# Performance work log

Measured on AMD Instinct MI355X. Metric: run time of the kernel, lower is better.

## Reference

```python
import jax, jax.numpy as jnp
import numpy as np

B, L, DM, E, N, R, S = 2, 1024, 512, 1024, 16, 32, 64
BN_SCALE = float(1.0 / np.sqrt(1.0 + 1e-5))  # eval-mode BatchNorm1d with default running stats


def _ssm(x, Wx, bx, Wdt, bdt, A_log, D):
    # x: [B,L,E] -> Mamba selective scan output [B,L,E]
    dbc = x @ Wx.T + bx                                   # [B,L,R+2N]
    delta = jax.nn.softplus(dbc[..., :R] @ Wdt.T + bdt)   # [B,L,E]
    Bm = dbc[..., R:R + N]                                # [B,L,N]
    Cm = dbc[..., R + N:]                                 # [B,L,N]
    A = -jnp.exp(A_log)                                   # [E,N]
    dA = jnp.exp(delta[..., None] * A)                    # [B,L,E,N]
    dBx = delta[..., None] * Bm[:, :, None, :] * x[..., None]

    def comb(c1, c2):
        a1, b1 = c1
        a2, b2 = c2
        return a1 * a2, b1 * a2 + b2

    _, h = jax.lax.associative_scan(comb, (dA, dBx), axis=1)  # [B,L,E,N]
    return jnp.einsum('blen,bln->ble', h, Cm) + D * x


def _gmask_idx(length, batch):
    ref = (length + 1) // 2
    idx = jnp.arange(length, dtype=jnp.float32)
    sigma = jnp.abs(idx - ref).mean()
    w = jnp.exp(-0.5 * (idx - ref) ** 2 / sigma ** 2)
    w = w / w.sum()
    return jnp.broadcast_to(w, (batch, length))


def _gmask_vec(seq):
    length = seq.shape[1]
    ref = seq[:, (length + 1) // 2, :]
    d = jnp.linalg.norm(seq - ref[:, None, :], axis=2)    # [B,L]
    sigma = d.mean(axis=1, keepdims=True)
    w = jnp.exp(-0.5 * (d / sigma) ** 2)
    return w / w.sum(axis=1, keepdims=True)


def _spatial_attn(x, w, b):
    # x: [B,L,C]; SpatialAttention: returns weighted map in [B,C,L] layout
    xt = jnp.swapaxes(x, 1, 2)                            # [B,C,L]
    fmap = (w[0] * xt.max(axis=1) + w[1] * xt.mean(axis=1) + b) * BN_SCALE
    wmap = jax.nn.sigmoid(jax.nn.relu(fmap))[:, None, :]  # [B,1,L]
    return xt * wmap                                      # [B,C,L]


def _forward(x, W_in_x, b_in_x, W_in_z, b_in_z, convf_w, convf_b, convb_w, convb_b,
             Wx_f, bx_f, Wdt_f, bdt_f, A_log_f, D_f,
             Wx_b, bx_b, Wdt_b, bdt_b, A_log_b, D_b,
             W_cat, b_cat, sa_w, sa_b, wA_f, wV_f,
             W_proj, b_proj, W_Bi, b_Bi, tf_w, tf_b, W_out, b_out):
    b_, l_, _ = x.shape
    xi = x @ W_in_x.T + b_in_x                            # [B,L,E]
    z = x @ W_in_z.T + b_in_z                             # [B,L,E]
    # depthwise conv1d with kernel_size=1 == per-channel affine
    x_f = jax.nn.silu(xi * convf_w + convf_b)
    x_b = jax.nn.silu(jnp.flip(xi, axis=1) * convb_w + convb_b)
    y_f = jnp.tanh(_ssm(x_f, Wx_f, bx_f, Wdt_f, bdt_f, A_log_f, D_f))
    y_b = jnp.tanh(_ssm(x_b, Wx_b, bx_b, Wdt_b, bdt_b, A_log_b, D_b))
    gi = _gmask_idx(l_, b_)
    mf = jax.nn.softmax(gi * _gmask_vec(y_f), axis=1)
    mb = jax.nn.softmax(gi * _gmask_vec(y_b), axis=1)
    y_cat = jnp.concatenate([y_f * mf[..., None],
                             y_b * jnp.flip(mb[..., None], axis=1)], axis=-1)
    y = y_cat @ W_cat.T + b_cat                           # [B,L,E]
    m = jax.nn.softmax(gi * _gmask_vec(y_cat), axis=1)
    y = y * m[..., None]
    yw = _spatial_attn(y, sa_w, sa_b)                     # [B,E,L]
    y = jnp.swapaxes(yw, 1, 2)                            # [B,L,E]
    # STL tokenizer (forward direction weights)
    Aw = jax.nn.softmax(jnp.swapaxes(y @ wA_f.T, 1, 2), axis=-1)  # [B,S,L]
    u = Aw @ (y @ wV_f)                                   # [B,S,E]
    # z branch: adaptive average pool L -> S (L % S == 0), then SiLU
    zp = jax.nn.silu(jnp.swapaxes(z, 1, 2).reshape(b_, E, S, l_ // S).mean(-1))
    zt = jnp.swapaxes(zp, 1, 2)                           # [B,S,E]
    # TokenFuser -- faithful to original's .view-based memory reinterpretation
    Y = (u.reshape(b_, E, S) @ W_proj.T + b_proj).reshape(b_, S, E)
    Bw = jax.nn.sigmoid(zt @ W_Bi.T + b_Bi)               # [B,S,S]
    BwY = Bw @ Y                                          # [B,S,E]
    xj = _spatial_attn(zt, tf_w, tf_b).reshape(b_, S, E)  # view (reshape), not transpose
    out = BwY + xj
    return jnp.tanh(out @ W_out.T + b_out)                # [B,S,DM]


def setup_inputs():
    ks = jax.random.split(jax.random.key(0), 24)
    g = lambda i, shape, s=0.02: jax.random.normal(ks[i], shape, dtype=jnp.float32) * s
    A_log = jnp.log(jnp.tile(jnp.arange(1, N + 1, dtype=jnp.float32), (E, 1)))
    return dict(
        x=jax.random.normal(ks[0], (B, L, DM), dtype=jnp.float32),
        W_in_x=g(1, (E, DM)), b_in_x=jnp.zeros((E,), jnp.float32),
        W_in_z=g(2, (E, DM)), b_in_z=jnp.zeros((E,), jnp.float32),
        convf_w=1.0 + g(3, (E,)), convf_b=jnp.zeros((E,), jnp.float32),
        convb_w=1.0 + g(4, (E,)), convb_b=jnp.zeros((E,), jnp.float32),
        Wx_f=g(5, (R + 2 * N, E)), bx_f=jnp.zeros((R + 2 * N,), jnp.float32),
        Wdt_f=g(6, (E, R)), bdt_f=jnp.full((E,), -4.0, jnp.float32),
        A_log_f=A_log, D_f=jnp.ones((E,), jnp.float32),
        Wx_b=g(7, (R + 2 * N, E)), bx_b=jnp.zeros((R + 2 * N,), jnp.float32),
        Wdt_b=g(8, (E, R)), bdt_b=jnp.full((E,), -4.0, jnp.float32),
        A_log_b=A_log, D_b=jnp.ones((E,), jnp.float32),
        W_cat=g(9, (E, 2 * E)), b_cat=jnp.zeros((E,), jnp.float32),
        sa_w=g(10, (2,), 0.5), sa_b=jnp.zeros((), jnp.float32),
        wA_f=g(11, (S, E), 0.05), wV_f=g(12, (E, E), 0.02),
        W_proj=g(13, (S, S), 0.1), b_proj=jnp.zeros((S,), jnp.float32),
        W_Bi=g(14, (S, E)), b_Bi=jnp.zeros((S,), jnp.float32),
        tf_w=g(15, (2,), 0.5), tf_b=jnp.zeros((), jnp.float32),
        W_out=g(16, (DM, E)), b_out=jnp.zeros((DM,), jnp.float32),
    )


def reference(x, W_in_x, b_in_x, W_in_z, b_in_z, convf_w, convf_b, convb_w, convb_b,
              Wx_f, bx_f, Wdt_f, bdt_f, A_log_f, D_f,
              Wx_b, bx_b, Wdt_b, bdt_b, A_log_b, D_b,
              W_cat, b_cat, sa_w, sa_b, wA_f, wV_f,
              W_proj, b_proj, W_Bi, b_Bi, tf_w, tf_b, W_out, b_out):
    return _forward(x, W_in_x, b_in_x, W_in_z, b_in_z, convf_w, convf_b, convb_w, convb_b,
                    Wx_f, bx_f, Wdt_f, bdt_f, A_log_f, D_f,
                    Wx_b, bx_b, Wdt_b, bdt_b, A_log_b, D_b,
                    W_cat, b_cat, sa_w, sa_b, wA_f, wV_f,
                    W_proj, b_proj, W_Bi, b_Bi, tf_w, tf_b, W_out, b_out)
```

## Files before the change

### kernel.cpp

```cpp
#include <hip/hip_runtime.h>
#include <math.h>

#define DEVI static __device__ __forceinline__

namespace {

constexpr float BN_SCALE_C = 0.9999950000374997f;

typedef __bf16 bf8v __attribute__((ext_vector_type(8)));
typedef float f4v __attribute__((ext_vector_type(4)));

DEVI float sigmoidf_(float x){ return 1.0f/(1.0f+expf(-x)); }
DEVI float siluf_(float x){ return x/(1.0f+expf(-x)); }
DEVI float softplusf_(float x){ return fmaxf(x,0.0f) + log1pf(__expf(-fabsf(x))); }

DEVI unsigned short f2bf(float f){
  union{float f; unsigned int u;} v; v.f=f;
  unsigned int r = v.u + 0x7fffu + ((v.u>>16)&1u);
  return (unsigned short)(r>>16);
}

DEVI float bredw_sum(float v, float* sh){
  #pragma unroll
  for (int o=32;o;o>>=1) v += __shfl_xor(v, o);
  __syncthreads();
  if ((threadIdx.x&63)==0) sh[threadIdx.x>>6] = v;
  __syncthreads();
  return sh[0]+sh[1]+sh[2]+sh[3];
}
DEVI float bredw_max(float v, float* sh){
  #pragma unroll
  for (int o=32;o;o>>=1) v = fmaxf(v, __shfl_xor(v, o));
  __syncthreads();
  if ((threadIdx.x&63)==0) sh[threadIdx.x>>6] = v;
  __syncthreads();
  return fmaxf(fmaxf(sh[0],sh[1]), fmaxf(sh[2],sh[3]));
}

DEVI void gld_lds16(const unsigned short* g, unsigned short* l){
  __builtin_amdgcn_global_load_lds(
      (const __attribute__((address_space(1))) unsigned int*)(g),
      (__attribute__((address_space(3))) unsigned int*)(l), 16, 0, 0);
}

DEVI void stage_tile64(const unsigned short* __restrict__ Ak,
                       const unsigned short* __restrict__ Bk,
                       size_t lda, size_t ldb,
                       unsigned short* As, unsigned short* Bs,
                       int w, int lane)
{
  #pragma unroll
  for (int i=0;i<2;++i){
    int seg = (w<<1) + i;
    int row = (seg<<3) + (lane>>3);
    int c   = (lane & 7) ^ (row & 7);
    gld_lds16(Ak + (size_t)row*lda + (c<<3), As + (seg<<9));
    gld_lds16(Bk + (size_t)row*ldb + (c<<3), Bs + (seg<<9));
  }
}

DEVI void gemm_core(const unsigned short* __restrict__ Ag,
                    const unsigned short* __restrict__ Bg,
                    size_t lda, size_t ldb, int ksteps,
                    unsigned short* As, unsigned short* Bs, f4v (&acc)[2][2])
{
  const int tid = threadIdx.x;
  const int lane = tid & 63, w = tid >> 6;
  const int wr = w >> 1, wc = w & 1;
  const int l15 = lane & 15, l4 = lane >> 4;

  int cur = 0;
  stage_tile64(Ag, Bg, lda, ldb, As, Bs, w, lane);
  asm volatile("s_waitcnt vmcnt(0)" ::: "memory");
  __syncthreads();
  for (int ks = 0; ks < ksteps; ++ks){
    unsigned short* Asc = As + (cur<<12);
    unsigned short* Bsc = Bs + (cur<<12);
    if (ks+1 < ksteps)
      stage_tile64(Ag + (size_t)(ks+1)*64, Bg + (size_t)(ks+1)*64, lda, ldb,
                   As + ((cur^1)<<12), Bs + ((cur^1)<<12), w, lane);
    #pragma unroll
    for (int kk=0;kk<2;++kk){
      int cb = (kk<<2) + l4;
      bf8v af[2], bfv[2];
      #pragma unroll
      for (int mi=0;mi<2;++mi){
        int row = (wr<<5)+(mi<<4)+l15;
        af[mi] = *(const bf8v*)(Asc + (row<<6) + ((cb^(row&7))<<3));
      }
      #pragma unroll
      for (int ni=0;ni<2;++ni){
        int row = (wc<<5)+(ni<<4)+l15;
        bfv[ni] = *(const bf8v*)(Bsc + (row<<6) + ((cb^(row&7))<<3));
      }
      #pragma unroll
      for (int mi=0;mi<2;++mi)
        #pragma unroll
        for (int ni=0;ni<2;++ni)
          acc[mi][ni] = __builtin_amdgcn_mfma_f32_16x16x32_bf16(af[mi], bfv[ni], acc[mi][ni], 0,0,0);
    }
    asm volatile("s_waitcnt vmcnt(0)" ::: "memory");
    __syncthreads();
    cur ^= 1;
  }
}

template<int EPI>
__global__ __launch_bounds__(256) void gemm_bf16_k(
    const unsigned short* __restrict__ A, const unsigned short* __restrict__ Bt,
    const float* __restrict__ bias, void* __restrict__ Cout,
    int N, int K,
    const unsigned short* __restrict__ Bt2, const float* __restrict__ bias2, long sC)
{
  __shared__ unsigned short As[8192], Bs[8192];
  float* Cf = (float*)Cout;
  if (Bt2 && blockIdx.z){ Bt = Bt2; bias = bias2; Cf += sC; }
  const int m0 = blockIdx.y<<6, n0 = blockIdx.x<<6;
  f4v acc[2][2] = {};
  gemm_core(A + (size_t)m0*K, Bt + (size_t)n0*K, K, K, K>>6, As, Bs, acc);
  const int lane = threadIdx.x & 63, w = threadIdx.x >> 6;
  const int wr = w>>1, wc = w&1, l15 = lane&15, l4 = lane>>4;
  #pragma unroll
  for (int mi=0;mi<2;++mi)
    #pragma unroll
    for (int ni=0;ni<2;++ni){
      int col = n0 + (wc<<5) + (ni<<4) + l15;
      float bv = bias ? bias[col] : 0.f;
      #pragma unroll
      for (int r=0;r<4;++r){
        int rowg = m0 + (wr<<5) + (mi<<4) + (l4<<2) + r;
        Cf[(size_t)rowg*N + col] = acc[mi][ni][r] + bv;
      }
    }
}

template<int EPI>
__global__ __launch_bounds__(256) void gemm_small_k(
    const unsigned short* __restrict__ A, const unsigned short* __restrict__ Bt,
    const float* __restrict__ b0, const float* __restrict__ b1,
    void* __restrict__ Cout, int N, int K, int mshift, long sB)
{
  __shared__ unsigned char smem[65536];
  unsigned short* AsAll = (unsigned short*)smem;
  unsigned short* BsAll = (unsigned short*)(smem + 32768);
  float* Lc = (float*)smem;

  const int tid = threadIdx.x;
  const int lane = tid & 63, w = tid >> 6;
  const int m0 = blockIdx.y<<6, n0 = blockIdx.x<<6;
  const unsigned short* Ab = A + (size_t)m0*K;
  const unsigned short* Bb = Bt + (size_t)(m0>>mshift)*sB + (size_t)n0*K;
  unsigned short* Asw = AsAll + (w<<12);
  unsigned short* Bsw = BsAll + (w<<12);
  const int kpw = K >> 2;
  const int nst = kpw >> 6;
  const int l15 = lane & 15, l4 = lane >> 4;
  const int srow8 = lane >> 3, sc = lane & 7;

  f4v acc[4][4] = {};
  for (int ks = 0; ks < nst; ++ks){
    const int kbase = w*kpw + (ks<<6);
    #pragma unroll
    for (int seg=0; seg<8; ++seg){
      int row = (seg<<3) + srow8;
      int c = sc ^ (row & 7);
      gld_lds16(Ab + (size_t)row*K + kbase + (c<<3), Asw + (seg<<9));
      gld_lds16(Bb + (size_t)row*K + kbase + (c<<3), Bsw + (seg<<9));
    }
    asm volatile("s_waitcnt vmcnt(0)" ::: "memory");
    #pragma unroll
    for (int kk=0; kk<2; ++kk){
      int cb = (kk<<2) + l4;
      bf8v af[4], bfv[4];
      #pragma unroll
      for (int mi=0;mi<4;++mi){
        int row = (mi<<4) + l15;
        af[mi] = *(const bf8v*)(Asw + (row<<6) + ((cb^(row&7))<<3));
      }
      #pragma unroll
      for (int ni=0;ni<4;++ni){
        int row = (ni<<4) + l15;
        bfv[ni] = *(const bf8v*)(Bsw + (row<<6) + ((cb^(row&7))<<3));
      }
      #pragma unroll
      for (int mi=0;mi<4;++mi)
        #pragma unroll
        for (int ni=0;ni<4;++ni)
          acc[mi][ni] = __builtin_amdgcn_mfma_f32_16x16x32_bf16(af[mi], bfv[ni], acc[mi][ni], 0,0,0);
    }
    __builtin_amdgcn_sched_barrier(0);
  }
  __syncthreads();
  #pragma unroll
  for (int mi=0;mi<4;++mi)
    #pragma unroll
    for (int ni=0;ni<4;++ni){
      int col = (ni<<4) + l15;
      #pragma unroll
      for (int r=0;r<4;++r){
// ... 62 lines not shown
    int tx = threadIdx.x & 31, ty = threadIdx.x >> 5;
    if (tb < 1024){
      int by = tb >> 5, bx = tb & 31;
      #pragma unroll
      for (int r=0;r<4;++r){
        int row = by*32 + ty + r*8;
        tsh[ty + r*8][tx] = wV[(long)row*1024 + bx*32 + tx];
      }
      __syncthreads();
      #pragma unroll
      for (int r=0;r<4;++r){
        int row = bx*32 + ty + r*8;
        wVT[(long)row*1024 + by*32 + tx] = f2bf(tsh[tx][ty + r*8]);
      }
    } else {
      int q = tb - 1024;
      int dir = q >> 5, bi = q & 31;
      const float* src = dir ? Wdt_b : Wdt_f;
      float* dst = WdtT + (dir<<15);
      #pragma unroll
      for (int r=0;r<4;++r){
        int row = bi*32 + ty + r*8;
        tsh[ty + r*8][tx] = src[(long)row*32 + tx];
      }
      __syncthreads();
      #pragma unroll
      for (int r=0;r<4;++r){
        int c = ty + r*8;
        dst[(long)c*1024 + bi*32 + tx] = tsh[tx][c];
      }
    }
    return;
  }
  int i = (blockIdx.x*256 + threadIdx.x)*4;
  const float* s; unsigned short* d;
  if (i < n0){ s = s0; d = d0; }
  else if ((i -= n0) < n1){ s = s1; d = d1; }
  else if ((i -= n1) < n2){ s = s2; d = d2; }
  else if ((i -= n2) < n3){ s = s3; d = d3; }
  else if ((i -= n3) < n4){ s = s4; d = d4; }
  else if ((i -= n4) < n5){ s = s5; d = d5; }
  else if ((i -= n5) < n6){ s = s6; d = d6; }
  else if ((i -= n6) < n7){ s = s7; d = d7; }
  else return;
  float4 v = *(const float4*)(s + i);
  union{ unsigned short u[4]; uint2 p; } o;
  o.u[0]=f2bf(v.x); o.u[1]=f2bf(v.y); o.u[2]=f2bf(v.z); o.u[3]=f2bf(v.w);
  *(uint2*)(d + i) = o.p;
}

__global__ __launch_bounds__(256) void convzt_k(const float* __restrict__ xi, const float* __restrict__ z,
    const float* __restrict__ cfw, const float* __restrict__ cfb,
    const float* __restrict__ cbw, const float* __restrict__ cbb,
    float* __restrict__ xf, float* __restrict__ xb, unsigned short* __restrict__ xfb_bf,
    float* __restrict__ ztb)
{
  int bx = blockIdx.x, t = threadIdx.x;
  if (bx < 2048){
    int base = (bx*256 + t) << 2;
    int e = base & 1023;
    int bl = base >> 10; int l = bl & 1023, b = bl >> 10;
    float4 cw = *(const float4*)(cfw + e);
    float4 cb = *(const float4*)(cfb + e);
    float4 xv = *(const float4*)(xi + base);
    float4 vf;
    vf.x = siluf_(fmaf(xv.x, cw.x, cb.x));
    vf.y = siluf_(fmaf(xv.y, cw.y, cb.y));
    vf.z = siluf_(fmaf(xv.z, cw.z, cb.z));
    vf.w = siluf_(fmaf(xv.w, cw.w, cb.w));
    *(float4*)(xf + base) = vf;
    union{unsigned short u[4]; uint2 p;} o;
    o.u[0]=f2bf(vf.x); o.u[1]=f2bf(vf.y); o.u[2]=f2bf(vf.z); o.u[3]=f2bf(vf.w);
    *(uint2*)(xfb_bf + base) = o.p;
    int jb = (((b<<10) + (1023-l))<<10) + e;
    float4 cw2 = *(const float4*)(cbw + e);
    float4 cb2 = *(const float4*)(cbb + e);
    float4 xw = *(const float4*)(xi + jb);
    float4 vb;
    vb.x = siluf_(fmaf(xw.x, cw2.x, cb2.x));
    vb.y = siluf_(fmaf(xw.y, cw2.y, cb2.y));
    vb.z = siluf_(fmaf(xw.z, cw2.z, cb2.z));
    vb.w = siluf_(fmaf(xw.w, cw2.w, cb2.w));
    *(float4*)(xb + base) = vb;
    union{unsigned short u[4]; uint2 p;} o2;
    o2.u[0]=f2bf(vb.x); o2.u[1]=f2bf(vb.y); o2.u[2]=f2bf(vb.z); o2.u[3]=f2bf(vb.w);
    *(uint2*)(xfb_bf + 2097152 + base) = o2.p;
  } else {
    int base = ((bx-2048)*256 + t) << 2;
    int e = base & 1023; int bs = base >> 10; int s = bs & 63; int b = bs >> 6;
    const float* zp = z + (((long)((b<<10)+(s<<4)))<<10) + e;
    float4 sm = {0.f,0.f,0.f,0.f};
    #pragma unroll
    for (int j=0;j<16;++j){
      float4 v = *(const float4*)(zp + ((long)j<<10));
      sm.x += v.x; sm.y += v.y; sm.z += v.z; sm.w += v.w;
    }
    float4 o;
    o.x = siluf_(sm.x*(1.f/16.f)); o.y = siluf_(sm.y*(1.f/16.f));
    o.z = siluf_(sm.z*(1.f/16.f)); o.w = siluf_(sm.w*(1.f/16.f));
    *(float4*)(ztb + base) = o;
  }
}

__global__ __launch_bounds__(256) void dbcdelta_k(
    const float* __restrict__ dbcF, const float* __restrict__ WdtT,
    const float* __restrict__ bdt_f, const float* __restrict__ bdt_b,
    float* __restrict__ delta)
{
  __shared__ float sdbc[8][64];
  const int t = threadIdx.x;
  const int r0 = blockIdx.x * 8;
  const int dir = r0 >> 11;
  const float* bdt = dir ? bdt_b : bdt_f;
  const float* WT  = WdtT + (dir<<15);
  for (int idx=t; idx<512; idx+=256){
    int r = idx>>6, c = idx&63;
    sdbc[r][c] = dbcF[(long)(r0+r)*64 + c];
  }
  __syncthreads();
  const int c0 = t << 2;
  float4 bv = *(const float4*)(bdt + c0);
  float4 acc[8];
  #pragma unroll
  for (int r=0;r<8;++r) acc[r] = bv;
  #pragma unroll
  for (int k=0;k<32;++k){
    float4 w = *(const float4*)(WT + (k<<10) + c0);
    #pragma unroll
    for (int r=0;r<8;++r){
      float a = sdbc[r][k];
      acc[r].x = fmaf(a, w.x, acc[r].x);
      acc[r].y = fmaf(a, w.y, acc[r].y);
      acc[r].z = fmaf(a, w.z, acc[r].z);
      acc[r].w = fmaf(a, w.w, acc[r].w);
    }
  }
  #pragma unroll
  for (int r=0;r<8;++r){
    float4 o;
    o.x = softplusf_(acc[r].x); o.y = softplusf_(acc[r].y);
    o.z = softplusf_(acc[r].z); o.w = softplusf_(acc[r].w);
    *(float4*)(delta + (long)(r0+r)*1024 + c0) = o;
  }
}

__global__ __launch_bounds__(256) void ssm_chunk_k(
    const float* __restrict__ xs0, const float* __restrict__ dl0,
    const float* __restrict__ dbc0, const float* __restrict__ A_log_f,
    const float* __restrict__ A_log_b,
    float* __restrict__ pA0, float* __restrict__ hend0)
{
  const int dir = blockIdx.y;
  const float* xs   = xs0  + (size_t)dir*2097152;
  const float* delta= dl0  + (size_t)dir*2097152;
  const float* dbc  = dbc0 + (size_t)dir*131072;
  const float* A_log= dir ? A_log_b : A_log_f;
  float* pA   = pA0   + (size_t)dir*1048576;
  float* hend = hend0 + (size_t)dir*1048576;

  __shared__ float sB[32][16];
  const int tid = threadIdx.x;
  const int lane = tid & 63, w = tid >> 6;
  const int le = lane & 31, half = lane >> 5;
  const int bc = blockIdx.x >> 3;
  const int b = bc >> 5, c = bc & 31;
  const int e = ((blockIdx.x & 7) << 7) + (w << 5) + le;
  for (int i=tid; i<512; i+=256){
    int l=i>>4, n=i&15;
    sB[l][n] = dbc[(((b<<10) + (c<<5) + l)<<6) + 32 + n];
  }
  __syncthreads();
  const int n0 = half << 3;
  float An[8];
  #pragma unroll
  for (int j=0;j<8;++j) An[j] = -__expf(A_log[(e<<4)+n0+j]);
  float h[8];
  #pragma unroll
  for (int j=0;j<8;++j) h[j]=0.0f;
  float ds = 0.f;
  long base = ((long)((b<<10) + (c<<5)))*1024 + e;
  for (int l=0;l<32;++l){
    float dl = delta[base + ((long)l<<10)];
    float xv = xs[base + ((long)l<<10)];
    float dx = dl*xv;
    ds += dl;
    #pragma unroll
    for (int j=0;j<8;++j){
      float a = __expf(dl*An[j]);
      h[j] = fmaf(a, h[j], dx*sB[l][n0+j]);
    }
  }
  long ob = ((long)((b<<5)+c)<<4)*1024 + e;
  #pragma unroll
  for (int j=0;j<8;++j){
    pA[ob + ((long)(n0+j)<<10)] = __expf(ds*An[j]);
    hend[ob + ((long)(n0+j)<<10)] = h[j];
  }
}

__global__ __launch_bounds__(256) void ssm_carry_k(
    const float* __restrict__ pA, const float* __restrict__ hend, float* __restrict__ Hc)
{
  int i = blockIdx.x*256 + threadIdx.x;
  int e = i & 1023, n = (i>>10)&15, b = (i>>14)&1, dir = (i>>15)&1;
  const float* pAd = pA   + (size_t)dir*1048576;
  const float* hd  = hend + (size_t)dir*1048576;
  float* Hd        = Hc   + (size_t)dir*1048576;
  float H = 0.f;
  long base = ((long)(b*512 + n))*1024 + e;
  for (int c=0;c<32;++c){
    long a = base + (long)c*16384;
    Hd[a] = H;
    H = fmaf(pAd[a], H, hd[a]);
  }
}

__global__ __launch_bounds__(256) void ssm_out_k(
    const float* __restrict__ xs0, const float* __restrict__ dl0,
    const float* __restrict__ dbc0, const float* __restrict__ A_log_f,
    const float* __restrict__ A_log_b, const float* __restrict__ Hc0,
    const float* __restrict__ D_f, const float* __restrict__ D_b,
    float* __restrict__ y0)
{
  const int dir = blockIdx.y;
  const float* xs   = xs0  + (size_t)dir*2097152;
  const float* delta= dl0  + (size_t)dir*2097152;
  const float* dbc  = dbc0 + (size_t)dir*131072;
  const float* A_log= dir ? A_log_b : A_log_f;
  const float* Hc   = Hc0 + (size_t)dir*1048576;
  const float* D    = dir ? D_b : D_f;
  float* y          = y0 + (size_t)dir*2097152;

  __shared__ float sB[32][16], sC[32][16];
  const int tid = threadIdx.x;
  const int lane = tid & 63, w = tid >> 6;
  const int le = lane & 31, half = lane >> 5;
  const int bc = blockIdx.x >> 3;
  const int b = bc >> 5, c = bc & 31;
  const int e = ((blockIdx.x & 7) << 7) + (w << 5) + le;
  for (int i=tid;i<512;i+=256){
    int l=i>>4, n=i&15;
    int bbase = ((b<<10)+(c<<5)+l)<<6;
    sB[l][n] = dbc[bbase+32+n];
    sC[l][n] = dbc[bbase+48+n];
  }
  __syncthreads();
  const int n0 = half << 3;
  float An[8], h[8];
  long ib = ((long)((b<<5)+c)<<4)*1024 + e;
  #pragma unroll
  for(int j=0;j<8;++j){
    An[j] = -__expf(A_log[(e<<4)+n0+j]);
    h[j] = Hc[ib+((long)(n0+j)<<10)];
  }
  const float Dv = D[e];
  long base = ((long)((b<<10)+(c<<5)))*1024 + e;
  for (int l=0;l<32;++l){
    float dl = delta[base+((long)l<<10)];
    float xv = xs[base+((long)l<<10)];
    float dx = dl*xv;
    float acc = half ? 0.f : Dv*xv;
    #pragma unroll
    for(int j=0;j<8;++j){
      float a = __expf(dl*An[j]);
      h[j] = fmaf(a,h[j],dx*sB[l][n0+j]);
      acc = fmaf(h[j], sC[l][n0+j], acc);
    }
    acc += __shfl_xor(acc, 32);
    if (!half) y[base+((long)l<<10)] = tanhf(acc);
  }
}

__global__ __launch_bounds__(256) void stats_k(const float* __restrict__ y,
    float* __restrict__ nrm, float* __restrict__ dotv)
{
  __shared__ float sh[4];
  int row = blockIdx.x;
  int rowref = (row & ~1023) + 512;
  const float4* rp  = (const float4*)(y + (long)row*1024);
  const float4* rf  = (const float4*)(y + (long)rowref*1024);
  float4 a = rp[threadIdx.x], r = rf[threadIdx.x];
  float sn = a.x*a.x + a.y*a.y + a.z*a.z + a.w*a.w;
  float sd = a.x*r.x + a.y*r.y + a.z*r.z + a.w*r.w;
  sn = bredw_sum(sn, sh);
  sd = bredw_sum(sd, sh);
  if (threadIdx.x==0){ nrm[row] = sn; dotv[row] = sd; }
}

DEVI void softmask(const float (&d)[4], const float (&gi)[4], float gsum,
                   float* sh, float (&m)[4])
{
  float s = d[0]+d[1]+d[2]+d[3];
  float sig = bredw_sum(s, sh) * (1.0f/1024.0f);
  float inv = 1.0f/sig;
  float w[4]; s = 0.f;
  #pragma unroll
  for (int i=0;i<4;++i){ float r = d[i]*inv; w[i] = __expf(-0.5f*r*r); s += w[i]; }
  float wsm = bredw_sum(s, sh);
  float sc = 1.0f/(wsm*gsum);
  float tv[4]; float mx = -1e30f;
  #pragma unroll
  for (int i=0;i<4;++i){ tv[i] = gi[i]*w[i]*sc; mx = fmaxf(mx, tv[i]); }
  mx = bredw_max(mx, sh);
  s = 0.f;
  #pragma unroll
  for (int i=0;i<4;++i){ tv[i] = __expf(tv[i]-mx); s += tv[i]; }
  float es = bredw_sum(s, sh);
  float ie = 1.0f/es;
  #pragma unroll
  for (int i=0;i<4;++i) m[i] = tv[i]*ie;
}

__global__ __launch_bounds__(256) void mask2_k(
    const float* __restrict__ nrm, const float* __restrict__ dotv,
    float* __restrict__ mfG, float* __restrict__ mbG, float* __restrict__ mvG)
{
  __shared__ float mfs[1024], mbs[1024], sh[4];
  const int b = blockIdx.x, t = threadIdx.x;
  const float nf512 = nrm[(b<<10)+512];
  const float nb512 = nrm[2048+(b<<10)+512];
  float gi[4], nf[4], pf[4], nb[4], pb[4];
  float gs = 0.f;
  #pragma unroll
  for (int i=0;i<4;++i){
    int l = t + (i<<8);
    float q = (float)(l-512) * (1.0f/256.0f);
    gi[i] = __expf(-0.5f*q*q); gs += gi[i];
    nf[i] = nrm[(b<<10)+l];      pf[i] = dotv[(b<<10)+l];
    nb[i] = nrm[2048+(b<<10)+l]; pb[i] = dotv[2048+(b<<10)+l];
  }
  float gsum = bredw_sum(gs, sh);
  float mf[4], mb[4], d[4];
  #pragma unroll
  for (int i=0;i<4;++i) d[i] = sqrtf(fmaxf(nf[i] - 2.f*pf[i] + nf512, 0.f));
  softmask(d, gi, gsum, sh, mf);
  #pragma unroll
  for (int i=0;i<4;++i) d[i] = sqrtf(fmaxf(nb[i] - 2.f*pb[i] + nb512, 0.f));
  softmask(d, gi, gsum, sh, mb);
  #pragma unroll
  for (int i=0;i<4;++i){
    int l = t + (i<<8);
    mfs[l] = mf[i]; mbs[l] = mb[i];
    mfG[(b<<10)+l] = mf[i]; mbG[(b<<10)+l] = mb[i];
  }
  __syncthreads();
  const float mf512 = mfs[512], mb511 = mbs[511];
  #pragma unroll
  for (int i=0;i<4;++i){
    int l = t + (i<<8);
    float mbf = mbs[1023-l];
    float dc2 = mf[i]*mf[i]*nf[i] - 2.f*mf[i]*mf512*pf[i] + mf512*mf512*nf512
              + mbf*mbf*nb[i]     - 2.f*mbf*mb511*pb[i]   + mb511*mb511*nb512;
    d[i] = sqrtf(fmaxf(dc2, 0.f));
  }
  float mv[4];
  softmask(d, gi, gsum, sh, mv);
  #pragma unroll
  for (int i=0;i<4;++i) mvG[(b<<10)+t+(i<<8)] = mv[i];
}

__global__ __launch_bounds__(256) void ycat_k(const float* __restrict__ yf, const float* __restrict__ yb,
    const float* __restrict__ mf, const float* __restrict__ mb, unsigned short* __restrict__ yc)
{
  int base = (blockIdx.x*256 + threadIdx.x) << 2;
  int e = base & 1023; int bl = base >> 10; int l = bl & 1023, b = bl >> 10;
  float mfv = mf[bl];
  float mbv = mb[(b<<10) + (1023-l)];
  float4 vf = *(const float4*)(yf + base);
  float4 vb = *(const float4*)(yb + base);
  long r = (long)bl*2048;
  union{unsigned short u[4]; uint2 p;} o;
  o.u[0]=f2bf(vf.x*mfv); o.u[1]=f2bf(vf.y*mfv); o.u[2]=f2bf(vf.z*mfv); o.u[3]=f2bf(vf.w*mfv);
  *(uint2*)(yc + r + e) = o.p;
  union{unsigned short u[4]; uint2 p;} o2;
  o2.u[0]=f2bf(vb.x*mbv); o2.u[1]=f2bf(vb.y*mbv); o2.u[2]=f2bf(vb.z*mbv); o2.u[3]=f2bf(vb.w*mbv);
  *(uint2*)(yc + r + 1024 + e) = o2.p;
}

__global__ __launch_bounds__(256) void rowscale_k(const float* __restrict__ y, const float* __restrict__ m,
    const float* __restrict__ sw, const float* __restrict__ sb, unsigned short* __restrict__ yo)
{
  __shared__ float sh[4];
  int row = blockIdx.x;
  float mv = m[row];
  float4 v = ((const float4*)(y + (long)row*1024))[threadIdx.x];
  v.x *= mv; v.y *= mv; v.z *= mv; v.w *= mv;
  float mx = fmaxf(fmaxf(v.x,v.y), fmaxf(v.z,v.w));
  float sm = v.x+v.y+v.z+v.w;
  float rmax = bredw_max(mx, sh);
  float rsum = bredw_sum(sm, sh);
  float fmap = (sw[0]*rmax + sw[1]*(rsum*(1.0f/1024.0f)) + sb[0])*BN_SCALE_C;
  float sc = sigmoidf_(fmaxf(fmap, 0.0f));
  union{unsigned short u[4]; uint2 p;} o;
  o.u[0]=f2bf(v.x*sc); o.u[1]=f2bf(v.y*sc); o.u[2]=f2bf(v.z*sc); o.u[3]=f2bf(v.w*sc);
  *(uint2*)(yo + (long)row*1024 + (threadIdx.x<<2)) = o.p;
}

__global__ __launch_bounds__(256) void awsmT_k(const float* __restrict__ yA,
    unsigned short* __restrict__ Aw,
    const unsigned short* __restrict__ src, unsigned short* __restrict__ dst)
{
  __shared__ float sh[4];
  __shared__ unsigned short tsh[32][33];
  if (blockIdx.x < 128){
    int bs = blockIdx.x; int b = bs >> 6, s = bs & 63;
    float v[4]; float mx=-1e30f;
    #pragma unroll
    for(int i=0;i<4;++i){
      int l = threadIdx.x+(i<<8);
      v[i] = yA[(long)((b<<10)+l)*64 + s];
      mx = fmaxf(mx, v[i]);
    }
    mx = bredw_max(mx, sh);
    float sm=0.0f;
    #pragma unroll
    for(int i=0;i<4;++i){ v[i]=__expf(v[i]-mx); sm+=v[i]; }
    sm = bredw_sum(sm, sh);
    float inv = 1.0f/sm;
    #pragma unroll
    for(int i=0;i<4;++i){ int l=threadIdx.x+(i<<8); Aw[(((b<<6)+s)<<10)+l] = f2bf(v[i]*inv); }
  } else {
    int tb = blockIdx.x - 128;
    size_t bo = (size_t)(tb>>10) << 20;
    int rem = tb & 1023;
    int by = rem >> 5, bx = rem & 31;
    int tx = threadIdx.x & 31, ty = threadIdx.x >> 5;
    #pragma unroll
    for (int r=0;r<4;++r){
// ... 96 lines not shown

}

extern "C" void kernel_launch(void* const* d_in, const int* in_sizes, int n_in,
                              void* d_out, int out_size, void* d_ws, size_t ws_size,
                              hipStream_t stream)
{
  (void)in_sizes; (void)n_in; (void)out_size; (void)ws_size;
  const float* x      = (const float*)d_in[0];
  const float* W_in_x = (const float*)d_in[1];
  const float* b_in_x = (const float*)d_in[2];
  const float* W_in_z = (const float*)d_in[3];
  const float* b_in_z = (const float*)d_in[4];
  const float* cfw    = (const float*)d_in[5];
  const float* cfb    = (const float*)d_in[6];
  const float* cbw    = (const float*)d_in[7];
  const float* cbb    = (const float*)d_in[8];
  const float* Wx_f   = (const float*)d_in[9];
  const float* bx_f   = (const float*)d_in[10];
  const float* Wdt_f  = (const float*)d_in[11];
  const float* bdt_f  = (const float*)d_in[12];
  const float* A_log_f= (const float*)d_in[13];
  const float* D_f    = (const float*)d_in[14];
  const float* Wx_b   = (const float*)d_in[15];
  const float* bx_b   = (const float*)d_in[16];
  const float* Wdt_b  = (const float*)d_in[17];
  const float* bdt_b  = (const float*)d_in[18];
  const float* A_log_b= (const float*)d_in[19];
  const float* D_b    = (const float*)d_in[20];
  const float* W_cat  = (const float*)d_in[21];
  const float* b_cat  = (const float*)d_in[22];
  const float* sa_w   = (const float*)d_in[23];
  const float* sa_b   = (const float*)d_in[24];
  const float* wA_f   = (const float*)d_in[25];
  const float* wV_f   = (const float*)d_in[26];
  const float* W_proj = (const float*)d_in[27];
  const float* b_proj = (const float*)d_in[28];
  const float* W_Bi   = (const float*)d_in[29];
  const float* b_Bi   = (const float*)d_in[30];
  const float* tf_w   = (const float*)d_in[31];
  const float* tf_b   = (const float*)d_in[32];
  const float* W_out  = (const float*)d_in[33];
  const float* b_out  = (const float*)d_in[34];
  float* out = (float*)d_out;
  float* ws  = (float*)d_ws;

  const size_t M1 = 1u<<20;
  float* xi = ws;
  float* pA = ws;
  unsigned short* ycat_bf = (unsigned short*)ws;
  float* z = ws + 2*M1;
  float* hend = ws + 2*M1;
  float* ybufF = ws + 2*M1;
  float* xf = ws + 4*M1;
  unsigned short* ybuf_bf = (unsigned short*)(ws + 4*M1);
  float* xb = ws + 6*M1;
  unsigned short* ybufT_bf = (unsigned short*)(ws + 6*M1);
  float* yf = ws + 8*M1;
  float* yb = ws + 10*M1;
  float* u2f = ws + 10*M1;
  unsigned short* xfxb_bf = (unsigned short*)(ws + 12*M1);
  float* deltaF = ws + 12*M1;
  unsigned short* x_bf = (unsigned short*)(ws + 17*M1);
  float* Hc = ws + 16*M1;
  float* dbcF = ws + 18*M1;
  size_t woff = 18*M1 + 262144;
  unsigned short* Winx_bf = (unsigned short*)(ws + woff); woff += 262144;
  unsigned short* Winz_bf = (unsigned short*)(ws + woff); woff += 262144;
  unsigned short* Wcat_bf = (unsigned short*)(ws + woff); woff += M1;
  unsigned short* wVT_bf  = (unsigned short*)(ws + woff); woff += 524288;
  unsigned short* wA_bf   = (unsigned short*)(ws + woff); woff += 32768;
  unsigned short* Wx_bf   = (unsigned short*)(ws + woff); woff += 65536;
  unsigned short* Wout_bf = (unsigned short*)(ws + woff); woff += 262144;
  float* WdtT = ws + woff; woff += 65536;
  float* ztb  = ws + woff; woff += 131072;
  float* nrm  = ws + woff; woff += 4096;
  float* dotv = ws + woff; woff += 4096;
  float* mfG  = ws + woff; woff += 2048;
  float* mbG  = ws + woff; woff += 2048;
  float* mvG  = ws + woff; woff += 2048;
  float* gz   = ws + woff; woff += 256;
  float* yA   = ws + woff; woff += 131072;
  unsigned short* Aw_bf = (unsigned short*)(ws + woff); woff += 65536;
  unsigned short* uR_bf = (unsigned short*)(ws + woff); woff += 65536;
  float* Yp   = ws + woff; woff += 131072;
  float* Bw   = ws + woff; woff += 8192;
  unsigned short* O_bf = (unsigned short*)(ws + woff); woff += 65536;

  dim3 blk(256);

  castall_k<<<5888,blk,0,stream>>>(x, x_bf, 1048576,
                                   W_in_x, Winx_bf, 524288,
                                   W_in_z, Winz_bf, 524288,
                                   W_cat, Wcat_bf, 2097152,
                                   wA_f, wA_bf, 65536,
                                   Wx_f, Wx_bf, 65536,
                                   Wx_b, Wx_bf + 65536, 65536,
                                   W_out, Wout_bf, 524288,
                                   wV_f, wVT_bf, Wdt_f, Wdt_b, WdtT);

  gemm_bf16_k<0><<<dim3(16,32,2),blk,0,stream>>>(x_bf, Winx_bf, b_in_x, xi, 1024, 512,
                                                 Winz_bf, b_in_z, (long)(2*M1));
  convzt_k<<<2176,blk,0,stream>>>(xi, z, cfw,cfb,cbw,cbb, xf, xb, xfxb_bf, ztb);

  gemm_small_k<0><<<dim3(1,64),blk,0,stream>>>(xfxb_bf, Wx_bf, bx_f, bx_b, dbcF,
                                               64, 1024, 11, 65536);
  dbcdelta_k<<<512,blk,0,stream>>>(dbcF, WdtT, bdt_f, bdt_b, deltaF);

  ssm_chunk_k<<<dim3(512,2),blk,0,stream>>>(xf, deltaF, dbcF, A_log_f, A_log_b, pA, hend);
  ssm_carry_k<<<256,blk,0,stream>>>(pA, hend, Hc);
  ssm_out_k<<<dim3(512,2),blk,0,stream>>>(xf, deltaF, dbcF, A_log_f, A_log_b, Hc, D_f, D_b, yf);

  stats_k<<<4096,blk,0,stream>>>(yf, nrm, dotv);
  mask2_k<<<2,blk,0,stream>>>(nrm, dotv, mfG, mbG, mvG);
  ycat_k<<<2048,blk,0,stream>>>(yf, yb, mfG, mbG, ycat_bf);

  gemm_bf16_k<0><<<dim3(16,32,1),blk,0,stream>>>(ycat_bf, Wcat_bf, b_cat, ybufF, 1024, 2048,
                                                 nullptr, nullptr, 0);
  rowscale_k<<<2048,blk,0,stream>>>(ybufF, mvG, sa_w, sa_b, ybuf_bf);

  gemm_small_k<0><<<dim3(1,32),blk,0,stream>>>(ybuf_bf, wA_bf, nullptr, nullptr, yA,
                                               64, 1024, 31, 0);
  awsmT_k<<<2176,blk,0,stream>>>(yA, Aw_bf, ybuf_bf, ybufT_bf);
  gemm_small_k<1><<<dim3(16,2),blk,0,stream>>>(Aw_bf, ybufT_bf, nullptr, nullptr, uR_bf,
                                               1024, 1024, 6, (long)M1);
  gemm_small_k<0><<<dim3(16,2),blk,0,stream>>>(uR_bf, wVT_bf, nullptr, nullptr, u2f,
                                               1024, 1024, 31, 0);

  upbw_k<<<384,blk,0,stream>>>(u2f, W_proj, b_proj, ztb, W_Bi, b_Bi, tf_w, tf_b, Yp, Bw, gz);
  o_k<<<128,blk,0,stream>>>(Bw, Yp, ztb, gz, O_bf);

  gemm_small_k<2><<<dim3(8,2),blk,0,stream>>>(O_bf, Wout_bf, b_out, nullptr, out,
                                              512, 1024, 31, 0);
}
```

Measured before the change: 209.8 us.

## Store SSM intermediates in bf16 and route big GEMMs through split-K kernel

Drops the fp32 copies of the conv outputs and reuses the bf16 xf/xb buffer in the scan kernels. Delta and the scan output y are now written in bf16, and the stats and concat kernels read bf16. This roughly halves the memory traffic of those bandwidth-bound kernels, at the cost of extra rounding error in delta and y. It also removes the double-buffered 64x64 GEMM and runs the input projections and W_cat GEMM on gemm_small_k with a z-dim weight switch, which changes the tiling and split-K behaviour for these large GEMMs.

```diff
diff --git a/kernel.cpp b/kernel.cpp
--- a/kernel.cpp
+++ b/kernel.cpp
@@ -19,6 +19,10 @@
   unsigned int r = v.u + 0x7fffu + ((v.u>>16)&1u);
   return (unsigned short)(r>>16);
 }
+DEVI float bf2f(unsigned short u){
+  union{unsigned int u; float f;} v; v.u = ((unsigned int)u)<<16;
+  return v.f;
+}
 
 DEVI float bredw_sum(float v, float* sh){
   #pragma unroll
@@ -43,108 +47,19 @@
       (__attribute__((address_space(3))) unsigned int*)(l), 16, 0, 0);
 }
 
-DEVI void stage_tile64(const unsigned short* __restrict__ Ak,
-                       const unsigned short* __restrict__ Bk,
-                       size_t lda, size_t ldb,
-                       unsigned short* As, unsigned short* Bs,
-                       int w, int lane)
-{
-  #pragma unroll
-  for (int i=0;i<2;++i){
-    int seg = (w<<1) + i;
-    int row = (seg<<3) + (lane>>3);
-    int c   = (lane & 7) ^ (row & 7);
-    gld_lds16(Ak + (size_t)row*lda + (c<<3), As + (seg<<9));
-    gld_lds16(Bk + (size_t)row*ldb + (c<<3), Bs + (seg<<9));
-  }
-}
-
-DEVI void gemm_core(const unsigned short* __restrict__ Ag,
-                    const unsigned short* __restrict__ Bg,
-                    size_t lda, size_t ldb, int ksteps,
-                    unsigned short* As, unsigned short* Bs, f4v (&acc)[2][2])
-{
-  const int tid = threadIdx.x;
-  const int lane = tid & 63, w = tid >> 6;
-  const int wr = w >> 1, wc = w & 1;
-  const int l15 = lane & 15, l4 = lane >> 4;
-
-  int cur = 0;
-  stage_tile64(Ag, Bg, lda, ldb, As, Bs, w, lane);
-  asm volatile("s_waitcnt vmcnt(0)" ::: "memory");
-  __syncthreads();
-  for (int ks = 0; ks < ksteps; ++ks){
-    unsigned short* Asc = As + (cur<<12);
-    unsigned short* Bsc = Bs + (cur<<12);
-    if (ks+1 < ksteps)
-      stage_tile64(Ag + (size_t)(ks+1)*64, Bg + (size_t)(ks+1)*64, lda, ldb,
-                   As + ((cur^1)<<12), Bs + ((cur^1)<<12), w, lane);
-    #pragma unroll
-    for (int kk=0;kk<2;++kk){
-      int cb = (kk<<2) + l4;
-      bf8v af[2], bfv[2];
-      #pragma unroll
-      for (int mi=0;mi<2;++mi){
-        int row = (wr<<5)+(mi<<4)+l15;
-        af[mi] = *(const bf8v*)(Asc + (row<<6) + ((cb^(row&7))<<3));
-      }
-      #pragma unroll
-      for (int ni=0;ni<2;++ni){
-        int row = (wc<<5)+(ni<<4)+l15;
-        bfv[ni] = *(const bf8v*)(Bsc + (row<<6) + ((cb^(row&7))<<3));
-      }
-      #pragma unroll
-      for (int mi=0;mi<2;++mi)
-        #pragma unroll
-        for (int ni=0;ni<2;++ni)
-          acc[mi][ni] = __builtin_amdgcn_mfma_f32_16x16x32_bf16(af[mi], bfv[ni], acc[mi][ni], 0,0,0);
-    }
-    asm volatile("s_waitcnt vmcnt(0)" ::: "memory");
-    __syncthreads();
-    cur ^= 1;
-  }
-}
-
-template<int EPI>
-__global__ __launch_bounds__(256) void gemm_bf16_k(
-    const unsigned short* __restrict__ A, const unsigned short* __restrict__ Bt,
-    const float* __restrict__ bias, void* __restrict__ Cout,
-    int N, int K,
-    const unsigned short* __restrict__ Bt2, const float* __restrict__ bias2, long sC)
-{
-  __shared__ unsigned short As[8192], Bs[8192];
-  float* Cf = (float*)Cout;
-  if (Bt2 && blockIdx.z){ Bt = Bt2; bias = bias2; Cf += sC; }
-  const int m0 = blockIdx.y<<6, n0 = blockIdx.x<<6;
-  f4v acc[2][2] = {};
-  gemm_core(A + (size_t)m0*K, Bt + (size_t)n0*K, K, K, K>>6, As, Bs, acc);
-  const int lane = threadIdx.x & 63, w = threadIdx.x >> 6;
-  const int wr = w>>1, wc = w&1, l15 = lane&15, l4 = lane>>4;
-  #pragma unroll
-  for (int mi=0;mi<2;++mi)
-    #pragma unroll
-    for (int ni=0;ni<2;++ni){
-      int col = n0 + (wc<<5) + (ni<<4) + l15;
-      float bv = bias ? bias[col] : 0.f;
-      #pragma unroll
-      for (int r=0;r<4;++r){
-        int rowg = m0 + (wr<<5) + (mi<<4) + (l4<<2) + r;
-        Cf[(size_t)rowg*N + col] = acc[mi][ni][r] + bv;
-      }
-    }
-}
-
 template<int EPI>
 __global__ __launch_bounds__(256) void gemm_small_k(
     const unsigned short* __restrict__ A, const unsigned short* __restrict__ Bt,
     const float* __restrict__ b0, const float* __restrict__ b1,
-    void* __restrict__ Cout, int N, int K, int mshift, long sB)
+    void* __restrict__ Cout, int N, int K, int mshift, long sB,
+    const unsigned short* __restrict__ Bt2, const float* __restrict__ bias2, long sC)
 {
   __shared__ unsigned char smem[65536];
   unsigned short* AsAll = (unsigned short*)smem;
   unsigned short* BsAll = (unsigned short*)(smem + 32768);
   float* Lc = (float*)smem;
 
+  if (Bt2 && blockIdx.z){ Bt = Bt2; b0 = bias2; Cout = (void*)((float*)Cout + sC); }
   const int tid = threadIdx.x;
   const int lane = tid & 63, w = tid >> 6;
   const int m0 = blockIdx.y<<6, n0 = blockIdx.x<<6;
@@ -313,8 +228,7 @@
 __global__ __launch_bounds__(256) void convzt_k(const float* __restrict__ xi, const float* __restrict__ z,
     const float* __restrict__ cfw, const float* __restrict__ cfb,
     const float* __restrict__ cbw, const float* __restrict__ cbb,
-    float* __restrict__ xf, float* __restrict__ xb, unsigned short* __restrict__ xfb_bf,
-    float* __restrict__ ztb)
+    unsigned short* __restrict__ xfb_bf, float* __restrict__ ztb)
 {
   int bx = blockIdx.x, t = threadIdx.x;
   if (bx < 2048){
@@ -324,27 +238,21 @@
     float4 cw = *(const float4*)(cfw + e);
     float4 cb = *(const float4*)(cfb + e);
     float4 xv = *(const float4*)(xi + base);
-    float4 vf;
-    vf.x = siluf_(fmaf(xv.x, cw.x, cb.x));
-    vf.y = siluf_(fmaf(xv.y, cw.y, cb.y));
-    vf.z = siluf_(fmaf(xv.z, cw.z, cb.z));
-    vf.w = siluf_(fmaf(xv.w, cw.w, cb.w));
-    *(float4*)(xf + base) = vf;
     union{unsigned short u[4]; uint2 p;} o;
-    o.u[0]=f2bf(vf.x); o.u[1]=f2bf(vf.y); o.u[2]=f2bf(vf.z); o.u[3]=f2bf(vf.w);
+    o.u[0]=f2bf(siluf_(fmaf(xv.x, cw.x, cb.x)));
+    o.u[1]=f2bf(siluf_(fmaf(xv.y, cw.y, cb.y)));
+    o.u[2]=f2bf(siluf_(fmaf(xv.z, cw.z, cb.z)));
+    o.u[3]=f2bf(siluf_(fmaf(xv.w, cw.w, cb.w)));
     *(uint2*)(xfb_bf + base) = o.p;
     int jb = (((b<<10) + (1023-l))<<10) + e;
     float4 cw2 = *(const float4*)(cbw + e);
     float4 cb2 = *(const float4*)(cbb + e);
     float4 xw = *(const float4*)(xi + jb);
-    float4 vb;
-    vb.x = siluf_(fmaf(xw.x, cw2.x, cb2.x));
-    vb.y = siluf_(fmaf(xw.y, cw2.y, cb2.y));
-    vb.z = siluf_(fmaf(xw.z, cw2.z, cb2.z));
-    vb.w = siluf_(fmaf(xw.w, cw2.w, cb2.w));
-    *(float4*)(xb + base) = vb;
     union{unsigned short u[4]; uint2 p;} o2;
-    o2.u[0]=f2bf(vb.x); o2.u[1]=f2bf(vb.y); o2.u[2]=f2bf(vb.z); o2.u[3]=f2bf(vb.w);
+    o2.u[0]=f2bf(siluf_(fmaf(xw.x, cw2.x, cb2.x)));
+    o2.u[1]=f2bf(siluf_(fmaf(xw.y, cw2.y, cb2.y)));
+    o2.u[2]=f2bf(siluf_(fmaf(xw.z, cw2.z, cb2.z)));
+    o2.u[3]=f2bf(siluf_(fmaf(xw.w, cw2.w, cb2.w)));
     *(uint2*)(xfb_bf + 2097152 + base) = o2.p;
   } else {
     int base = ((bx-2048)*256 + t) << 2;
@@ -366,7 +274,7 @@
 __global__ __launch_bounds__(256) void dbcdelta_k(
     const float* __restrict__ dbcF, const float* __restrict__ WdtT,
     const float* __restrict__ bdt_f, const float* __restrict__ bdt_b,
-    float* __restrict__ delta)
+    unsigned short* __restrict__ delta)
 {
   __shared__ float sdbc[8][64];
   const int t = threadIdx.x;
@@ -398,22 +306,24 @@
   }
   #pragma unroll
   for (int r=0;r<8;++r){
-    float4 o;
-    o.x = softplusf_(acc[r].x); o.y = softplusf_(acc[r].y);
-    o.z = softplusf_(acc[r].z); o.w = softplusf_(acc[r].w);
-    *(float4*)(delta + (long)(r0+r)*1024 + c0) = o;
+    union{unsigned short u[4]; uint2 p;} o;
+    o.u[0] = f2bf(softplusf_(acc[r].x));
+    o.u[1] = f2bf(softplusf_(acc[r].y));
+    o.u[2] = f2bf(softplusf_(acc[r].z));
+    o.u[3] = f2bf(softplusf_(acc[r].w));
+    *(uint2*)(delta + (long)(r0+r)*1024 + c0) = o.p;
   }
 }
 
 __global__ __launch_bounds__(256) void ssm_chunk_k(
-    const float* __restrict__ xs0, const float* __restrict__ dl0,
+    const unsigned short* __restrict__ xs0, const unsigned short* __restrict__ dl0,
     const float* __restrict__ dbc0, const float* __restrict__ A_log_f,
     const float* __restrict__ A_log_b,
     float* __restrict__ pA0, float* __restrict__ hend0)
 {
   const int dir = blockIdx.y;
-  const float* xs   = xs0  + (size_t)dir*2097152;
-  const float* delta= dl0  + (size_t)dir*2097152;
+  const unsigned short* xs   = xs0 + (size_t)dir*2097152;
+  const unsigned short* delta= dl0 + (size_t)dir*2097152;
   const float* dbc  = dbc0 + (size_t)dir*131072;
   const float* A_log= dir ? A_log_b : A_log_f;
   float* pA   = pA0   + (size_t)dir*1048576;
@@ -441,8 +351,8 @@
   float ds = 0.f;
   long base = ((long)((b<<10) + (c<<5)))*1024 + e;
   for (int l=0;l<32;++l){
-    float dl = delta[base + ((long)l<<10)];
-    float xv = xs[base + ((long)l<<10)];
+    float dl = bf2f(delta[base + ((long)l<<10)]);
+    float xv = bf2f(xs[base + ((long)l<<10)]);
     float dx = dl*xv;
     ds += dl;
     #pragma unroll
@@ -477,20 +387,20 @@
 }
 
 __global__ __launch_bounds__(256) void ssm_out_k(
-    const float* __restrict__ xs0, const float* __restrict__ dl0,
+    const unsigned short* __restrict__ xs0, const unsigned short* __restrict__ dl0,
     const float* __restrict__ dbc0, const float* __restrict__ A_log_f,
     const float* __restrict__ A_log_b, const float* __restrict__ Hc0,
     const float* __restrict__ D_f, const float* __restrict__ D_b,
-    float* __restrict__ y0)
+    unsigned short* __restrict__ y0)
 {
   const int dir = blockIdx.y;
-  const float* xs   = xs0  + (size_t)dir*2097152;
-  const float* delta= dl0  + (size_t)dir*2097152;
+  const unsigned short* xs   = xs0 + (size_t)dir*2097152;
+  const unsigned short* delta= dl0 + (size_t)dir*2097152;
   const float* dbc  = dbc0 + (size_t)dir*131072;
   const float* A_log= dir ? A_log_b : A_log_f;
   const float* Hc   = Hc0 + (size_t)dir*1048576;
   const float* D    = dir ? D_b : D_f;
-  float* y          = y0 + (size_t)dir*2097152;
+  unsigned short* y = y0 + (size_t)dir*2097152;
 
   __shared__ float sB[32][16], sC[32][16];
   const int tid = threadIdx.x;
@@ -517,8 +427,8 @@
   const float Dv = D[e];
   long base = ((long)((b<<10)+(c<<5)))*1024 + e;
   for (int l=0;l<32;++l){
-    float dl = delta[base+((long)l<<10)];
-    float xv = xs[base+((long)l<<10)];
+    float dl = bf2f(delta[base+((long)l<<10)]);
+    float xv = bf2f(xs[base+((long)l<<10)]);
     float dx = dl*xv;
     float acc = half ? 0.f : Dv*xv;
     #pragma unroll
@@ -528,21 +438,25 @@
       acc = fmaf(h[j], sC[l][n0+j], acc);
     }
     acc += __shfl_xor(acc, 32);
-    if (!half) y[base+((long)l<<10)] = tanhf(acc);
-  }
-}
-
-__global__ __launch_bounds__(256) void stats_k(const float* __restrict__ y,
+    if (!half) y[base+((long)l<<10)] = f2bf(tanhf(acc));
+  }
+}
+
+__global__ __launch_bounds__(256) void stats_k(const unsigned short* __restrict__ y,
     float* __restrict__ nrm, float* __restrict__ dotv)
 {
   __shared__ float sh[4];
   int row = blockIdx.x;
   int rowref = (row & ~1023) + 512;
-  const float4* rp  = (const float4*)(y + (long)row*1024);
-  const float4* rf  = (const float4*)(y + (long)rowref*1024);
-  float4 a = rp[threadIdx.x], r = rf[threadIdx.x];
-  float sn = a.x*a.x + a.y*a.y + a.z*a.z + a.w*a.w;
-  float sd = a.x*r.x + a.y*r.y + a.z*r.z + a.w*r.w;
+  const uint2* rp = (const uint2*)(y + (long)row*1024);
+  const uint2* rf = (const uint2*)(y + (long)rowref*1024);
+  uint2 av = rp[threadIdx.x], rv = rf[threadIdx.x];
+  float a0 = bf2f((unsigned short)(av.x&0xffff)), a1 = bf2f((unsigned short)(av.x>>16));
+  float a2 = bf2f((unsigned short)(av.y&0xffff)), a3 = bf2f((unsigned short)(av.y>>16));
+  float r0 = bf2f((unsigned short)(rv.x&0xffff)), r1 = bf2f((unsigned short)(rv.x>>16));
+  float r2 = bf2f((unsigned short)(rv.y&0xffff)), r3 = bf2f((unsigned short)(rv.y>>16));
+  float sn = a0*a0 + a1*a1 + a2*a2 + a3*a3;
+  float sd = a0*r0 + a1*r1 + a2*r2 + a3*r3;
   sn = bredw_sum(sn, sh);
   sd = bredw_sum(sd, sh);
   if (threadIdx.x==0){ nrm[row] = sn; dotv[row] = sd; }
@@ -620,21 +534,27 @@
   for (int i=0;i<4;++i) mvG[(b<<10)+t+(i<<8)] = mv[i];
 }
 
-__global__ __launch_bounds__(256) void ycat_k(const float* __restrict__ yf, const float* __restrict__ yb,
+__global__ __launch_bounds__(256) void ycat_k(const unsigned short* __restrict__ yall,
     const float* __restrict__ mf, const float* __restrict__ mb, unsigned short* __restrict__ yc)
 {
   int base = (blockIdx.x*256 + threadIdx.x) << 2;
   int e = base & 1023; int bl = base >> 10; int l = bl & 1023, b = bl >> 10;
   float mfv = mf[bl];
   float mbv = mb[(b<<10) + (1023-l)];
-  float4 vf = *(const float4*)(yf + base);
-  float4 vb = *(const float4*)(yb + base);
+  uint2 vf = *(const uint2*)(yall + base);
+  uint2 vb = *(const uint2*)(yall + 2097152 + base);
   long r = (long)bl*2048;
   union{unsigned short u[4]; uint2 p;} o;
-  o.u[0]=f2bf(vf.x*mfv); o.u[1]=f2bf(vf.y*mfv); o.u[2]=f2bf(vf.z*mfv); o.u[3]=f2bf(vf.w*mfv);
+  o.u[0]=f2bf(bf2f((unsigned short)(vf.x&0xffff))*mfv);
+  o.u[1]=f2bf(bf2f((unsigned short)(vf.x>>16))*mfv);
+  o.u[2]=f2bf(bf2f((unsigned short)(vf.y&0xffff))*mfv);
+  o.u[3]=f2bf(bf2f((unsigned short)(vf.y>>16))*mfv);
   *(uint2*)(yc + r + e) = o.p;
   union{unsigned short u[4]; uint2 p;} o2;
-  o2.u[0]=f2bf(vb.x*mbv); o2.u[1]=f2bf(vb.y*mbv); o2.u[2]=f2bf(vb.z*mbv); o2.u[3]=f2bf(vb.w*mbv);
+  o2.u[0]=f2bf(bf2f((unsigned short)(vb.x&0xffff))*mbv);
+  o2.u[1]=f2bf(bf2f((unsigned short)(vb.x>>16))*mbv);
+  o2.u[2]=f2bf(bf2f((unsigned short)(vb.y&0xffff))*mbv);
+  o2.u[3]=f2bf(bf2f((unsigned short)(vb.y>>16))*mbv);
   *(uint2*)(yc + r + 1024 + e) = o2.p;
 }
 
@@ -837,15 +757,12 @@
   float* z = ws + 2*M1;
   float* hend = ws + 2*M1;
   float* ybufF = ws + 2*M1;
-  float* xf = ws + 4*M1;
   unsigned short* ybuf_bf = (unsigned short*)(ws + 4*M1);
-  float* xb = ws + 6*M1;
   unsigned short* ybufT_bf = (unsigned short*)(ws + 6*M1);
-  float* yf = ws + 8*M1;
-  float* yb = ws + 10*M1;
+  unsigned short* y_bf = (unsigned short*)(ws + 8*M1);
   float* u2f = ws + 10*M1;
   unsigned short* xfxb_bf = (unsigned short*)(ws + 12*M1);
-  float* deltaF = ws + 12*M1;
+  unsigned short* delta_bf = (unsigned short*)(ws + 14*M1);
   unsigned short* x_bf = (unsigned short*)(ws + 17*M1);
   float* Hc = ws + 16*M1;
   float* dbcF = ws + 18*M1;
@@ -884,37 +801,38 @@
                                    W_out, Wout_bf, 524288,
                                    wV_f, wVT_bf, Wdt_f, Wdt_b, WdtT);
 
-  gemm_bf16_k<0><<<dim3(16,32,2),blk,0,stream>>>(x_bf, Winx_bf, b_in_x, xi, 1024, 512,
-                                                 Winz_bf, b_in_z, (long)(2*M1));
-  convzt_k<<<2176,blk,0,stream>>>(xi, z, cfw,cfb,cbw,cbb, xf, xb, xfxb_bf, ztb);
-
-  gemm_small_k<0><<<dim3(1,64),blk,0,stream>>>(xfxb_bf, Wx_bf, bx_f, bx_b, dbcF,
-                                               64, 1024, 11, 65536);
-  dbcdelta_k<<<512,blk,0,stream>>>(dbcF, WdtT, bdt_f, bdt_b, deltaF);
-
-  ssm_chunk_k<<<dim3(512,2),blk,0,stream>>>(xf, deltaF, dbcF, A_log_f, A_log_b, pA, hend);
+  gemm_small_k<0><<<dim3(16,32,2),blk,0,stream>>>(x_bf, Winx_bf, b_in_x, nullptr, xi,
+                                                  1024, 512, 31, 0,
+                                                  Winz_bf, b_in_z, (long)(2*M1));
+  convzt_k<<<2176,blk,0,stream>>>(xi, z, cfw,cfb,cbw,cbb, xfxb_bf, ztb);
+
+  gemm_small_k<0><<<dim3(1,64,1),blk,0,stream>>>(xfxb_bf, Wx_bf, bx_f, bx_b, dbcF,
+                                                 64, 1024, 11, 65536, nullptr, nullptr, 0);
+  dbcdelta_k<<<512,blk,0,stream>>>(dbcF, WdtT, bdt_f, bdt_b, delta_bf);
+
+  ssm_chunk_k<<<dim3(512,2),blk,0,stream>>>(xfxb_bf, delta_bf, dbcF, A_log_f, A_log_b, pA, hend);
   ssm_carry_k<<<256,blk,0,stream>>>(pA, hend, Hc);
-  ssm_out_k<<<dim3(512,2),blk,0,stream>>>(xf, deltaF, dbcF, A_log_f, A_log_b, Hc, D_f, D_b, yf);
-
-  stats_k<<<4096,blk,0,stream>>>(yf, nrm, dotv);
+  ssm_out_k<<<dim3(512,2),blk,0,stream>>>(xfxb_bf, delta_bf, dbcF, A_log_f, A_log_b, Hc, D_f, D_b, y_bf);
+
+  stats_k<<<4096,blk,0,stream>>>(y_bf, nrm, dotv);
   mask2_k<<<2,blk,0,stream>>>(nrm, dotv, mfG, mbG, mvG);
-  ycat_k<<<2048,blk,0,stream>>>(yf, yb, mfG, mbG, ycat_bf);
-
-  gemm_bf16_k<0><<<dim3(16,32,1),blk,0,stream>>>(ycat_bf, Wcat_bf, b_cat, ybufF, 1024, 2048,
-                                                 nullptr, nullptr, 0);
+  ycat_k<<<2048,blk,0,stream>>>(y_bf, mfG, mbG, ycat_bf);
+
+  gemm_small_k<0><<<dim3(16,32,1),blk,0,stream>>>(ycat_bf, Wcat_bf, b_cat, nullptr, ybufF,
+                                                  1024, 2048, 31, 0, nullptr, nullptr, 0);
   rowscale_k<<<2048,blk,0,stream>>>(ybufF, mvG, sa_w, sa_b, ybuf_bf);
 
-  gemm_small_k<0><<<dim3(1,32),blk,0,stream>>>(ybuf_bf, wA_bf, nullptr, nullptr, yA,
-                                               64, 1024, 31, 0);
+  gemm_small_k<0><<<dim3(1,32,1),blk,0,stream>>>(ybuf_bf, wA_bf, nullptr, nullptr, yA,
+                                                 64, 1024, 31, 0, nullptr, nullptr, 0);
   awsmT_k<<<2176,blk,0,stream>>>(yA, Aw_bf, ybuf_bf, ybufT_bf);
-  gemm_small_k<1><<<dim3(16,2),blk,0,stream>>>(Aw_bf, ybufT_bf, nullptr, nullptr, uR_bf,
-                                               1024, 1024, 6, (long)M1);
-  gemm_small_k<0><<<dim3(16,2),blk,0,stream>>>(uR_bf, wVT_bf, nullptr, nullptr, u2f,
-                                               1024, 1024, 31, 0);
+  gemm_small_k<1><<<dim3(16,2,1),blk,0,stream>>>(Aw_bf, ybufT_bf, nullptr, nullptr, uR_bf,
+                                                 1024, 1024, 6, (long)M1, nullptr, nullptr, 0);
+  gemm_small_k<0><<<dim3(16,2,1),blk,0,stream>>>(uR_bf, wVT_bf, nullptr, nullptr, u2f,
+                                                 1024, 1024, 31, 0, nullptr, nullptr, 0);
 
   upbw_k<<<384,blk,0,stream>>>(u2f, W_proj, b_proj, ztb, W_Bi, b_Bi, tf_w, tf_b, Yp, Bw, gz);
   o_k<<<128,blk,0,stream>>>(Bw, Yp, ztb, gz, O_bf);
 
-  gemm_small_k<2><<<dim3(8,2),blk,0,stream>>>(O_bf, Wout_bf, b_out, nullptr, out,
-                                              512, 1024, 31, 0);
-}
+  gemm_small_k<2><<<dim3(8,2,1),blk,0,stream>>>(O_bf, Wout_bf, b_out, nullptr, out,
+                                                512, 1024, 31, 0, nullptr, nullptr, 0);
+}
```

After: 207.5 us. No clear change (-1.1%).
